# Optimization experiments

Measured on AMD Instinct MI355X. Metric: run time of the kernel, lower is better.

The kernel has to match this reference:

```python
import jax, jax.numpy as jnp
import numpy as np
from jax import lax

EPS = 1e-5
GROUPS = 16


def group_norm(x, gamma, beta, g=GROUPS, eps=EPS):
    B, C, H, W = x.shape
    xr = x.reshape(B, g, C // g, H, W)
    mu = xr.mean(axis=(2, 3, 4), keepdims=True)
    var = xr.var(axis=(2, 3, 4), keepdims=True)
    xn = ((xr - mu) / jnp.sqrt(var + eps)).reshape(B, C, H, W)
    return xn * gamma[None, :, None, None] + beta[None, :, None, None]


def silu(x):
    return x * jax.nn.sigmoid(x)


def recurrence(a, b, c, d, x, axis):
    # h_t = a_t*h_{t-1} + b_t*x_t ; y_t = c_t*h_t + d_t*x_t, scanned along `axis`.
    mv = lambda t: jnp.moveaxis(t, axis, 0)
    def step(h, inp):
        at, bt, ct, dt, xt = inp
        h = at * h + bt * xt
        return h, ct * h + dt * xt
    xs = tuple(map(mv, (a, b, c, d, x)))
    h0 = jnp.zeros_like(xs[4][0])
    _, ys = lax.scan(step, h0, xs)
    return jnp.moveaxis(ys, 0, axis)


def dir_scan(x, wd, bd, axis, flip):
    # Conv1d(c,4c,1) over the scan sequence == pointwise channel linear on NCHW.
    xin = jnp.flip(x, axis) if flip else x
    coeff = jnp.einsum('oc,bchw->bohw', wd, xin) + bd[None, :, None, None]
    C = x.shape[1]
    a, b, c, d = (coeff[:, i * C:(i + 1) * C] for i in range(4))
    a = jax.nn.sigmoid(a)
    y = recurrence(a, b, c, d, xin, axis)
    return jnp.flip(y, axis) if flip else y


def setup_inputs() -> dict:
    key = jax.random.key(0)
    ks = jax.random.split(key, 10)
    B, C, H, W = 4, 128, 128, 128
    s = 1.0 / np.sqrt(C)
    inp = {
        'x': jax.random.normal(ks[0], (B, C, H, W), jnp.float32),
        'w_in': jax.random.normal(ks[1], (C, C), jnp.float32) * s,
        'gn1_gamma': jnp.ones((C,), jnp.float32),
        'gn1_beta': jnp.zeros((C,), jnp.float32),
        'w_gate': jax.random.normal(ks[2], (C, C), jnp.float32) * s,
        'b_gate': jax.random.normal(ks[3], (C,), jnp.float32) * 0.1,
        'dyn_w': jax.random.normal(ks[4], (4, 4 * C, C), jnp.float32) * s,
        'dyn_b': jax.random.normal(ks[5], (4, 4 * C), jnp.float32) * 0.1,
        'dw_kernel': jax.random.normal(ks[6], (C, 1, 3, 3), jnp.float32) * (1.0 / 3.0),
        'w_out': jax.random.normal(ks[7], (C, C), jnp.float32) * s,
        'gn2_gamma': jnp.ones((C,), jnp.float32),
        'gn2_beta': jnp.zeros((C,), jnp.float32),
    }
    return inp


def reference(x, w_in, gn1_gamma, gn1_beta, w_gate, b_gate, dyn_w, dyn_b,
              dw_kernel, w_out, gn2_gamma, gn2_beta):
    C = x.shape[1]
    # in_proj: 1x1 conv (no bias) -> GroupNorm -> SiLU
    xp = jnp.einsum('oc,bchw->bohw', w_in, x)
    xp = silu(group_norm(xp, gn1_gamma, gn1_beta))
    # 4-directional dynamic selective scans
    y_lr = dir_scan(xp, dyn_w[0], dyn_b[0], axis=3, flip=False)
    y_rl = dir_scan(xp, dyn_w[1], dyn_b[1], axis=3, flip=True)
    y_tb = dir_scan(xp, dyn_w[2], dyn_b[2], axis=2, flip=False)
    y_bt = dir_scan(xp, dyn_w[3], dyn_b[3], axis=2, flip=True)
    fused = 0.25 * (y_lr + y_rl + y_tb + y_bt)
    # gate: 1x1 conv + bias -> sigmoid, applied to projected x
    gate = jax.nn.sigmoid(jnp.einsum('oc,bchw->bohw', w_gate, xp)
                          + b_gate[None, :, None, None])
    z = fused * gate
    # out_proj: depthwise 3x3 -> 1x1 conv -> GroupNorm -> SiLU
    z = lax.conv_general_dilated(z, dw_kernel, (1, 1), ((1, 1), (1, 1)),
                                 feature_group_count=C,
                                 dimension_numbers=('NCHW', 'OIHW', 'NCHW'))
    z = jnp.einsum('oc,bchw->bohw', w_out, z)
    return silu(group_norm(z, gn2_gamma, gn2_beta))
```

## Files before the change

### kernel.cpp

```cpp
#include <hip/hip_runtime.h>
#include <math.h>

#define B_ 4
#define C_ 128
#define HW_ 16384
#define P_ 65536
#define S_ 8388608
#define CPG 8

typedef unsigned short u16;
typedef __attribute__((ext_vector_type(8))) short short8;
typedef __attribute__((ext_vector_type(4))) float f32x4;

__device__ __forceinline__ float sigmoidf_(float x){ return 1.f/(1.f+__expf(-x)); }
__device__ __forceinline__ float siluf_(float x){ return x*sigmoidf_(x); }
__device__ __forceinline__ u16 f2bf(float f){
  unsigned x = __float_as_uint(f);
  return (u16)((x + 0x7fffu + ((x >> 16) & 1u)) >> 16);
}
__device__ __forceinline__ float b2f(u16 u){ return __uint_as_float(((unsigned)u) << 16); }

__global__ __launch_bounds__(256) void prep_kernel(const float* __restrict__ dyn_w,
    const float* __restrict__ dyn_b, const float* __restrict__ w_gate,
    const float* __restrict__ w_out, const float* __restrict__ w_in,
    u16* __restrict__ wfrag, float* __restrict__ bperm, u16* __restrict__ wgbf,
    u16* __restrict__ wobf, u16* __restrict__ wibf, float* __restrict__ stats)
{
  int idx = blockIdx.x*256 + threadIdx.x;
  if (idx < 262144) {
    int e = idx & 7, lane = (idx >> 3) & 63, kk = (idx >> 9) & 3;
    int ct = (idx >> 11) & 31, d = idx >> 16;
    int m = lane & 15, kg = lane >> 4;
    int col = ct*16 + m;
    int c = col >> 2, f = col & 3;
    int k = kk*32 + kg*8 + e;
    wfrag[idx] = f2bf(dyn_w[(size_t)((d*512) + f*128 + c)*128 + k]);
  } else if (idx < 264192) {
    int i2 = idx - 262144;
    int op = i2 & 511, d = i2 >> 9;
    bperm[i2] = dyn_b[d*512 + (op & 3)*128 + (op >> 2)];
  } else if (idx < 280576) {
    wgbf[idx - 264192] = f2bf(w_gate[idx - 264192]);
  } else if (idx < 296960) {
    wobf[idx - 280576] = f2bf(w_out[idx - 280576]);
  } else if (idx < 313344) {
    wibf[idx - 296960] = f2bf(w_in[idx - 296960]);
  } else if (idx < 313600) {
    stats[idx - 313344] = 0.f;
  }
}

__global__ __launch_bounds__(256) void xpose(const float* __restrict__ x,
    u16* __restrict__ xT)
{
  __shared__ u16 tile[32*132];
  int b = blockIdx.y;
  int p0 = blockIdx.x << 5;
  int t = threadIdx.x;
  const float* xb = x + ((size_t)b << 21);
  #pragma unroll
  for (int i = 0; i < 16; ++i) {
    int idx = i*256 + t;
    int c = idx >> 5, pp = idx & 31;
    tile[pp*132 + c] = f2bf(xb[(size_t)c*HW_ + p0 + pp]);
  }
  __syncthreads();
  u16* ob = xT + ((size_t)b << 21) + ((size_t)p0 << 7);
  #pragma unroll
  for (int i = 0; i < 2; ++i) {
    int slot = i*256 + t;
    int pp = slot >> 4, j = slot & 15;
    uint2 v0 = *(const uint2*)((const char*)tile + pp*264 + j*16);
    uint2 v1 = *(const uint2*)((const char*)tile + pp*264 + j*16 + 8);
    uint4 o; o.x = v0.x; o.y = v0.y; o.z = v1.x; o.w = v1.y;
    *(uint4*)(ob + (pp << 7) + (j << 3)) = o;
  }
}

template<int BIAS, int SIG>
__global__ __launch_bounds__(256) void mfma_nt128(const u16* __restrict__ X,
    const u16* __restrict__ Wm, const float* __restrict__ bias, u16* __restrict__ Out)
{
  __shared__ __align__(16) u16 st[64*136];
  int t = threadIdx.x;
  int wv = t >> 6, lane = t & 63;
  int m = lane & 15, kg = lane >> 4;
  int pt = blockIdx.x << 6;

  short8 Af[4][4];
  #pragma unroll
  for (int rt = 0; rt < 4; ++rt) {
    const u16* ar = X + ((size_t)(pt + rt*16 + m) << 7) + kg*8;
    #pragma unroll
    for (int kk = 0; kk < 4; ++kk)
      Af[rt][kk] = *(const short8*)(ar + kk*32);
  }
  #pragma unroll
  for (int ct2 = 0; ct2 < 2; ++ct2) {
    int ot = wv*32 + ct2*16;
    const u16* wr = Wm + ((size_t)(ot + m) << 7) + kg*8;
    short8 Bf[4];
    #pragma unroll
    for (int kk = 0; kk < 4; ++kk)
      Bf[kk] = *(const short8*)(wr + kk*32);
    f32x4 acc[4];
    #pragma unroll
    for (int rt = 0; rt < 4; ++rt) acc[rt] = (f32x4){0.f,0.f,0.f,0.f};
    #pragma unroll
    for (int rt = 0; rt < 4; ++rt)
      #pragma unroll
      for (int kk = 0; kk < 4; ++kk)
        acc[rt] = __builtin_amdgcn_mfma_f32_16x16x32_bf16(Af[rt][kk], Bf[kk], acc[rt], 0, 0, 0);
    float bv = BIAS ? bias[ot + m] : 0.f;
    #pragma unroll
    for (int rt = 0; rt < 4; ++rt) {
      #pragma unroll
      for (int r = 0; r < 4; ++r) {
        float v = acc[rt][r] + bv;
        if (SIG) v = sigmoidf_(v);
        st[(rt*16 + kg*4 + r)*136 + ot + m] = f2bf(v);
      }
    }
  }
  __syncthreads();
  #pragma unroll
  for (int i = 0; i < 4; ++i) {
    int slot = i*256 + t;
    int row = slot >> 4, j = slot & 15;
    short8 v = *(const short8*)(st + row*136 + (j << 3));
    *(short8*)(Out + ((size_t)(pt + row) << 7) + (j << 3)) = v;
  }
}

#define PRODUCE(NT, bufv, chunkv)  do { \
  int posg_ = (chunkv)*16 + m; int swp_ = (posg_ & 7) << 4; \
  short8 Bfr[4]; \
  _Pragma("unroll") for (int kk = 0; kk < 4; ++kk) \
    Bfr[kk] = *(const short8*)((char*)xs + posg_*256 + (((kk<<6)+(kg<<4)) ^ swp_)); \
  _Pragma("unroll") for (int ti = 0; ti < NT; ++ti) { \
    f32x4 acc = (f32x4){0.f,0.f,0.f,0.f}; \
    _Pragma("unroll") for (int kk = 0; kk < 4; ++kk) \
      acc = __builtin_amdgcn_mfma_f32_16x16x32_bf16(Af[ti][kk], Bfr[kk], acc, 0, 0, 0); \
    int colL_ = (tbase + ti)*16 + (kg<<2); \
    unsigned lo_ = (unsigned)f2bf(acc[0]) | ((unsigned)f2bf(acc[1])<<16); \
    unsigned hi_ = (unsigned)f2bf(acc[2]) | ((unsigned)f2bf(acc[3])<<16); \
    int byte_ = (((bufv)*2 + dw)<<14) + (m<<10) + ((colL_<<1) ^ ((m&7)<<4)); \
    *(uint2*)((char*)cs + byte_) = make_uint2(lo_, hi_); \
  } } while(0)

#define SCAN_STEP(s) { \
  float ar = b2f((u16)(cw[s].x & 0xffffu)) + bv.x; \
  float br = b2f((u16)(cw[s].x >> 16)) + bv.y; \
  float cr = b2f((u16)(cw[s].y & 0xffffu)) + bv.z; \
  float dr = b2f((u16)(cw[s].y >> 16)) + bv.w; \
  float aa = sigmoidf_(ar); \
  h = aa*h + br*xf[s]; \
  yv[s] = cr*h + dr*xf[s]; }

template<int AXISW, int PART>
__global__ __launch_bounds__(512, 2) void scan_fused(const u16* __restrict__ Abf,
    const u16* __restrict__ Wf, const float* __restrict__ bias,
    u16* __restrict__ fusedP)
{
  __shared__ __align__(16) u16 xs[128*128];
  __shared__ __align__(16) u16 cs[2][2][16*512];
  __shared__ __align__(16) u16 ysL[128*128];
  int line = blockIdx.x;
  int b = line >> 7, l = line & 127;
  int t = threadIdx.x;
  int wv = t >> 6, lane = t & 63;
  int m = lane & 15, kg = lane >> 4;
  int dw = (wv >> 1) & 1;

  #pragma unroll
  for (int i = 0; i < 4; ++i) {
    int idx = i*512 + t;
    int pos = idx >> 4, j = idx & 15;
    size_t row = AXISW ? ((size_t)(b<<14) + (l<<7) + pos)
                       : ((size_t)(b<<14) + (pos<<7) + l);
    short8 v = *(const short8*)(Abf + (row<<7) + (j<<3));
    int byte = pos*256 + ((j*16) ^ ((pos&7)<<4));
    *(short8*)((char*)xs + byte) = v;
  }

  if (wv < 4) {
    int tbase = (wv & 1) * 4;
    short8 Af[4][4];
    #pragma unroll
    for (int ti = 0; ti < 4; ++ti)
      #pragma unroll
      for (int kk = 0; kk < 4; ++kk)
        Af[ti][kk] = *(const short8*)(Wf + (size_t)(((dw*32 + tbase + ti)*4 + kk)*64 + lane)*8);
    __syncthreads();
    PRODUCE(4, 0, dw ? 7 : 0);
    __syncthreads();

    int sd = dw;
    int sc = ((wv & 1) << 6) + lane;
    float4 bv = *(const float4*)(bias + (sd << 9) + (sc << 2));
    float h = 0.f;

    #pragma unroll 1
    for (int k = 0; k < 8; ++k) {
      if (k < 7) PRODUCE(4, (k+1)&1, dw ? (6-k) : (k+1));
      int chunk = sd ? (7-k) : k;
      int csb = (((k&1)*2 + sd) << 14);
      uint2 cw[16];
      #pragma unroll
      for (int s = 0; s < 16; ++s)
        cw[s] = *(const uint2*)((char*)cs + csb + (s<<10) + ((sc<<3) ^ ((s&7)<<4)));
      float xf[16];
      #pragma unroll
      for (int s = 0; s < 16; ++s) {
        int pos = (chunk<<4) + s;
        xf[s] = b2f(*(const u16*)((char*)xs + pos*256 + ((sc<<1) ^ ((s&7)<<4))));
      }
      float yv[16];
      __builtin_amdgcn_s_setprio(1);
      if (sd == 0) {
        #pragma unroll
        for (int s = 0; s < 16; ++s) SCAN_STEP(s)
      } else {
        #pragma unroll
        for (int s = 15; s >= 0; --s) SCAN_STEP(s)
      }
      __builtin_amdgcn_s_setprio(0);
      u16* yrow = ysL + (chunk << 11) + sc;
      if (k <= 3) {
        #pragma unroll
        for (int s = 0; s < 16; ++s) yrow[s << 7] = f2bf(0.25f*yv[s]);
      } else {
        #pragma unroll
        for (int s = 0; s < 16; ++s) {
          float o = b2f(yrow[s << 7]);
          yrow[s << 7] = f2bf(o + 0.25f*yv[s]);
        }
      }
      __syncthreads();
    }
  } else {
    int tbase = 8 + (wv & 1) * 12;
    short8 Af[12][4];
    #pragma unroll
    for (int ti = 0; ti < 12; ++ti)
      #pragma unroll
      for (int kk = 0; kk < 4; ++kk)
        Af[ti][kk] = *(const short8*)(Wf + (size_t)(((dw*32 + tbase + ti)*4 + kk)*64 + lane)*8);
    __syncthreads();
    PRODUCE(12, 0, dw ? 7 : 0);
    __syncthreads();
    #pragma unroll 1
    for (int k = 0; k < 8; ++k) {
      if (k < 7) PRODUCE(12, (k+1)&1, dw ? (6-k) : (k+1));
      __syncthreads();
    }
  }

  #pragma unroll
  for (int r = 0; r < 4; ++r) {
    int slot = r*512 + t;
    int pos = slot >> 4, j = slot & 15;
    short8 v = *(const short8*)(ysL + (pos << 7) + (j << 3));
    size_t rowg = AXISW ? ((size_t)(b<<14) + (l<<7) + pos)
                        : ((size_t)(b<<14) + (pos<<7) + l);
    u16* op = fusedP + (rowg << 7) + (j << 3);
    if (PART) {
      short8 o = *(const short8*)op;
      short8 rr;
      #pragma unroll
      for (int i = 0; i < 8; ++i) rr[i] = (short)f2bf(b2f((u16)v[i]) + b2f((u16)o[i]));
      *(short8*)op = rr;
    } else {
      *(short8*)op = v;
    }
  }
}

__global__ __launch_bounds__(256) void gn_stats_bf(const u16* __restrict__ X,
    float* __restrict__ stats)
{
  int bg = blockIdx.x, chunk = blockIdx.y;
  int b = bg >> 4, g = bg & 15;
  int t = threadIdx.x;
  int c = t & 7, pr = t >> 3;
  const u16* base = X + ((size_t)b << 21) + (g << 3) + c;
  int p0 = chunk << 10;
  float s = 0.f, s2 = 0.f;
  for (int i = 0; i < 32; ++i) {
    float v = b2f(base[(size_t)(p0 + (i << 5) + pr) << 7]);
    s += v; s2 += v*v;
  }
  #pragma unroll
  for (int off = 32; off; off >>= 1) { s += __shfl_down(s, off); s2 += __shfl_down(s2, off); }
  __shared__ float ls[8];
  int wv = t >> 6, lane = t & 63;
  if (lane == 0) { ls[wv] = s; ls[4 + wv] = s2; }
  __syncthreads();
  if (t == 0) {
    atomicAdd(&stats[bg], ls[0]+ls[1]+ls[2]+ls[3]);
    atomicAdd(&stats[64+bg], ls[4]+ls[5]+ls[6]+ls[7]);
  }
}

__global__ __launch_bounds__(256) void gn_apply(const u16* __restrict__ X,
    const float* __restrict__ stats, const float* __restrict__ gamma,
    const float* __restrict__ beta, u16* __restrict__ Xb)
{
  int i4 = blockIdx.x*256 + threadIdx.x;
  size_t base = (size_t)i4 << 2;
  int c4 = (int)(base & 127);
  size_t p = base >> 7;
  int b = (int)(p >> 14);
  int g = c4 >> 3;
  const float cnt = (float)(CPG*HW_);
  float mu = stats[b*16+g]/cnt;
  float var = stats[64+b*16+g]/cnt - mu*mu;
  float rs = rsqrtf(var + 1e-5f);
  ushort4 v = *(const ushort4*)(X + base);
  ushort4 o;
  o.x = f2bf(siluf_((b2f(v.x)-mu)*rs*gamma[c4+0]+beta[c4+0]));
  o.y = f2bf(siluf_((b2f(v.y)-mu)*rs*gamma[c4+1]+beta[c4+1]));
  o.z = f2bf(siluf_((b2f(v.z)-mu)*rs*gamma[c4+2]+beta[c4+2]));
  o.w = f2bf(siluf_((b2f(v.w)-mu)*rs*gamma[c4+3]+beta[c4+3]));
  *(ushort4*)(Xb + base) = o;
}

__global__ __launch_bounds__(256) void dwconv(const u16* __restrict__ Z,
    const u16* __restrict__ G, const float* __restrict__ K9, u16* __restrict__ Outp)
{
  __shared__ float kk[1152];
  int t = threadIdx.x;
  for (int i = t; i < 1152; i += 256) kk[i] = K9[i];
  __syncthreads();
  int i4 = blockIdx.x*256 + t;
  size_t base = (size_t)i4 << 2;
  int c0 = (int)(base & 127);
  size_t p = base >> 7;
  int w = (int)(p & 127), h = (int)((p >> 7) & 127), b = (int)(p >> 14);
  float4 acc = make_float4(0.f,0.f,0.f,0.f);
  #pragma unroll
  for (int di = 0; di < 3; ++di) {
    int hy = h + di - 1;
    if ((unsigned)hy > 127u) continue;
    #pragma unroll
    for (int dj = 0; dj < 3; ++dj) {
      int wx = w + dj - 1;
      if ((unsigned)wx > 127u) continue;
      size_t p2 = ((size_t)b << 14) + (hy << 7) + wx;
      ushort4 zv = *(const ushort4*)(Z + (p2 << 7) + c0);
      ushort4 gv = *(const ushort4*)(G + (p2 << 7) + c0);
      int o = di*3 + dj;
      acc.x += b2f(zv.x) * b2f(gv.x) * kk[c0*9 + o];
      acc.y += b2f(zv.y) * b2f(gv.y) * kk[(c0+1)*9 + o];
      acc.z += b2f(zv.z) * b2f(gv.z) * kk[(c0+2)*9 + o];
      acc.w += b2f(zv.w) * b2f(gv.w) * kk[(c0+3)*9 + o];
    }
  }
  ushort4 ov;
  ov.x = f2bf(acc.x); ov.y = f2bf(acc.y); ov.z = f2bf(acc.z); ov.w = f2bf(acc.w);
  *(ushort4*)(Outp + base) = ov;
}

__global__ __launch_bounds__(256) void gn_final(const u16* __restrict__ Z,
    const float* __restrict__ stats, const float* __restrict__ gamma,
    const float* __restrict__ beta, float* __restrict__ out)
{
  __shared__ float ls[32][129];
  int w0 = blockIdx.x << 5, hh = blockIdx.y, b = blockIdx.z;
  size_t p0 = ((size_t)b << 14) + (hh << 7) + w0;
  int t = threadIdx.x;
  const float cnt = (float)(CPG*HW_);
  #pragma unroll
  for (int i = 0; i < 4; ++i) {
    int l = t + i*256;
    int row = l >> 5, c4 = (l & 31) << 2;
    ushort4 v = *(const ushort4*)(Z + ((p0 + row) << 7) + c4);
    int g = c4 >> 3;
    float mu = stats[b*16+g]/cnt;
    float var = stats[64+b*16+g]/cnt - mu*mu;
    float rs = rsqrtf(var + 1e-5f);
    float vals[4] = {b2f(v.x), b2f(v.y), b2f(v.z), b2f(v.w)};
    #pragma unroll
    for (int j = 0; j < 4; ++j) {
      float nv = (vals[j]-mu)*rs*gamma[c4+j] + beta[c4+j];
      ls[row][c4+j] = siluf_(nv);
    }
  }
  __syncthreads();
  int ww = t & 31, c0 = t >> 5;
  #pragma unroll
  for (int cc = c0; cc < 128; cc += 8) {
    out[(((size_t)(b*128 + cc)) << 14) + (hh << 7) + (w0 + ww)] = ls[ww][cc];
  }
}

extern "C" void kernel_launch(void* const* d_in, const int* in_sizes, int n_in,
                              void* d_out, int out_size, void* d_ws, size_t ws_size,
                              hipStream_t stream)
{
  (void)in_sizes; (void)n_in; (void)out_size; (void)ws_size;
  const float* x      = (const float*)d_in[0];
  const float* w_in   = (const float*)d_in[1];
  const float* g1g    = (const float*)d_in[2];
  const float* g1b    = (const float*)d_in[3];
  const float* w_gate = (const float*)d_in[4];
  const float* b_gate = (const float*)d_in[5];
  const float* dyn_w  = (const float*)d_in[6];
  const float* dyn_b  = (const float*)d_in[7];
  const float* dwk    = (const float*)d_in[8];
  const float* w_out  = (const float*)d_in[9];
  const float* g2g    = (const float*)d_in[10];
  const float* g2b    = (const float*)d_in[11];
  float* out = (float*)d_out;

  char* p = (char*)d_ws;
  u16*   xT     = (u16*)p;              p += (size_t)S_*2;
  u16*   xpr    = (u16*)p;              p += (size_t)S_*2;
  u16*   Abf    = (u16*)p;              p += (size_t)S_*2;
  u16*   fusedP = (u16*)p;              p += (size_t)S_*2;
  u16*   Gbf    = (u16*)p;              p += (size_t)S_*2;
  u16*   wfrag  = (u16*)p;              p += (size_t)262144*2;
  u16*   wgbf   = (u16*)p;              p += (size_t)16384*2;
  u16*   wobf   = (u16*)p;              p += (size_t)16384*2;
  u16*   wibf   = (u16*)p;              p += (size_t)16384*2;
  float* bperm  = (float*)p;            p += (size_t)2048*4;
  float* stats  = (float*)p;            p += (size_t)256*4;
  u16*   Zdw    = xT;
  u16*   Zout   = xpr;

  prep_kernel<<<1225, 256, 0, stream>>>(dyn_w, dyn_b, w_gate, w_out, w_in,
                                        wfrag, bperm, wgbf, wobf, wibf, stats);
  xpose<<<dim3(512, 4), 256, 0, stream>>>(x, xT);
  mfma_nt128<0,0><<<1024, 256, 0, stream>>>(xT, wibf, nullptr, xpr);
  gn_stats_bf<<<dim3(64, 16), 256, 0, stream>>>(xpr, stats);
  gn_apply<<<8192, 256, 0, stream>>>(xpr, stats, g1g, g1b, Abf);

  scan_fused<1,0><<<512, 512, 0, stream>>>(Abf, wfrag, bperm, fusedP);
  scan_fused<0,1><<<512, 512, 0, stream>>>(Abf, wfrag + 131072, bperm + 1024, fusedP);

  mfma_nt128<1,1><<<1024, 256, 0, stream>>>(Abf, wgbf, b_gate, Gbf);
  dwconv<<<8192, 256, 0, stream>>>(fusedP, Gbf, dwk, Zdw);
  mfma_nt128<0,0><<<1024, 256, 0, stream>>>(Zdw, wobf, nullptr, Zout);
  gn_stats_bf<<<dim3(64, 16), 256, 0, stream>>>(Zout, stats + 128);
  gn_final<<<dim3(4, 128, 4), 256, 0, stream>>>(Zout, stats + 128, g2g, g2b, out);
}
```

Before: 236.2 us.

## Fuse input transpose into in-proj MFMA and vectorize GroupNorm stats reduction

Removes the separate xpose kernel. The in-projection GEMM now reads the fp32 NCHW input directly, converts it to bf16 in registers, and builds its MFMA A fragments from strided channel loads. This drops one full bf16 intermediate write and read plus a kernel launch. GroupNorm statistics now use contiguous 16-byte loads over position-major data with per-group shuffle and shared-atomic reduction, replacing strided scalar loads. The strided fp32 gathers in the in-proj kernel may coalesce poorly across lanes.

```diff
diff --git a/kernel.cpp b/kernel.cpp
--- a/kernel.cpp
+++ b/kernel.cpp
@@ -50,30 +50,61 @@
   }
 }
 
-__global__ __launch_bounds__(256) void xpose(const float* __restrict__ x,
-    u16* __restrict__ xT)
-{
-  __shared__ u16 tile[32*132];
-  int b = blockIdx.y;
-  int p0 = blockIdx.x << 5;
-  int t = threadIdx.x;
+__global__ __launch_bounds__(256) void mfma_inproj(const float* __restrict__ x,
+    const u16* __restrict__ Wm, u16* __restrict__ Out)
+{
+  __shared__ __align__(16) u16 st[64*136];
+  int t = threadIdx.x;
+  int wv = t >> 6, lane = t & 63;
+  int m = lane & 15, kg = lane >> 4;
+  int pt = blockIdx.x << 6;
+  int b = blockIdx.x >> 8;
+  int hw0 = (blockIdx.x & 255) << 6;
   const float* xb = x + ((size_t)b << 21);
-  #pragma unroll
-  for (int i = 0; i < 16; ++i) {
-    int idx = i*256 + t;
-    int c = idx >> 5, pp = idx & 31;
-    tile[pp*132 + c] = f2bf(xb[(size_t)c*HW_ + p0 + pp]);
-  }
-  __syncthreads();
-  u16* ob = xT + ((size_t)b << 21) + ((size_t)p0 << 7);
-  #pragma unroll
-  for (int i = 0; i < 2; ++i) {
+
+  short8 Af[4][4];
+  #pragma unroll
+  for (int rt = 0; rt < 4; ++rt) {
+    int pos = hw0 + rt*16 + m;
+    #pragma unroll
+    for (int kk = 0; kk < 4; ++kk) {
+      short8 f;
+      #pragma unroll
+      for (int e = 0; e < 8; ++e)
+        f[e] = (short)f2bf(xb[(size_t)(kk*32 + kg*8 + e)*HW_ + pos]);
+      Af[rt][kk] = f;
+    }
+  }
+  #pragma unroll
+  for (int ct2 = 0; ct2 < 2; ++ct2) {
+    int ot = wv*32 + ct2*16;
+    const u16* wr = Wm + ((size_t)(ot + m) << 7) + kg*8;
+    short8 Bf[4];
+    #pragma unroll
+    for (int kk = 0; kk < 4; ++kk)
+      Bf[kk] = *(const short8*)(wr + kk*32);
+    f32x4 acc[4];
+    #pragma unroll
+    for (int rt = 0; rt < 4; ++rt) acc[rt] = (f32x4){0.f,0.f,0.f,0.f};
+    #pragma unroll
+    for (int rt = 0; rt < 4; ++rt)
+      #pragma unroll
+      for (int kk = 0; kk < 4; ++kk)
+        acc[rt] = __builtin_amdgcn_mfma_f32_16x16x32_bf16(Af[rt][kk], Bf[kk], acc[rt], 0, 0, 0);
+    #pragma unroll
+    for (int rt = 0; rt < 4; ++rt) {
+      #pragma unroll
+      for (int r = 0; r < 4; ++r)
+        st[(rt*16 + kg*4 + r)*136 + ot + m] = f2bf(acc[rt][r]);
+    }
+  }
+  __syncthreads();
+  #pragma unroll
+  for (int i = 0; i < 4; ++i) {
     int slot = i*256 + t;
-    int pp = slot >> 4, j = slot & 15;
-    uint2 v0 = *(const uint2*)((const char*)tile + pp*264 + j*16);
-    uint2 v1 = *(const uint2*)((const char*)tile + pp*264 + j*16 + 8);
-    uint4 o; o.x = v0.x; o.y = v0.y; o.z = v1.x; o.w = v1.y;
-    *(uint4*)(ob + (pp << 7) + (j << 3)) = o;
+    int row = slot >> 4, j = slot & 15;
+    short8 v = *(const short8*)(st + row*136 + (j << 3));
+    *(short8*)(Out + ((size_t)(pt + row) << 7) + (j << 3)) = v;
   }
 }
 
@@ -279,27 +310,26 @@
 __global__ __launch_bounds__(256) void gn_stats_bf(const u16* __restrict__ X,
     float* __restrict__ stats)
 {
-  int bg = blockIdx.x, chunk = blockIdx.y;
-  int b = bg >> 4, g = bg & 15;
-  int t = threadIdx.x;
-  int c = t & 7, pr = t >> 3;
-  const u16* base = X + ((size_t)b << 21) + (g << 3) + c;
-  int p0 = chunk << 10;
-  float s = 0.f, s2 = 0.f;
-  for (int i = 0; i < 32; ++i) {
-    float v = b2f(base[(size_t)(p0 + (i << 5) + pr) << 7]);
-    s += v; s2 += v*v;
-  }
-  #pragma unroll
-  for (int off = 32; off; off >>= 1) { s += __shfl_down(s, off); s2 += __shfl_down(s2, off); }
-  __shared__ float ls[8];
-  int wv = t >> 6, lane = t & 63;
-  if (lane == 0) { ls[wv] = s; ls[4 + wv] = s2; }
-  __syncthreads();
-  if (t == 0) {
-    atomicAdd(&stats[bg], ls[0]+ls[1]+ls[2]+ls[3]);
-    atomicAdd(&stats[64+bg], ls[4]+ls[5]+ls[6]+ls[7]);
-  }
+  int b = blockIdx.x, chunk = blockIdx.y;
+  const u16* base = X + ((size_t)b << 21) + ((size_t)chunk << 15);
+  int t = threadIdx.x;
+  float s = 0.f, q = 0.f;
+  #pragma unroll 4
+  for (int it = 0; it < 16; ++it) {
+    short8 v = *(const short8*)(base + it*2048 + t*8);
+    #pragma unroll
+    for (int e = 0; e < 8; ++e) { float f = b2f((u16)v[e]); s += f; q += f*f; }
+  }
+  s += __shfl_xor(s, 16); q += __shfl_xor(q, 16);
+  s += __shfl_xor(s, 32); q += __shfl_xor(q, 32);
+  __shared__ float sg[32];
+  if (t < 32) sg[t] = 0.f;
+  __syncthreads();
+  int lane = t & 63;
+  if (lane < 16) { atomicAdd(&sg[lane], s); atomicAdd(&sg[16 + lane], q); }
+  __syncthreads();
+  if (t < 16) atomicAdd(&stats[b*16 + t], sg[t]);
+  else if (t < 32) atomicAdd(&stats[64 + b*16 + (t - 16)], sg[t]);
 }
 
 __global__ __launch_bounds__(256) void gn_apply(const u16* __restrict__ X,
@@ -414,7 +444,7 @@
   float* out = (float*)d_out;
 
   char* p = (char*)d_ws;
-  u16*   xT     = (u16*)p;              p += (size_t)S_*2;
+  u16*   Zbuf   = (u16*)p;              p += (size_t)S_*2;
   u16*   xpr    = (u16*)p;              p += (size_t)S_*2;
   u16*   Abf    = (u16*)p;              p += (size_t)S_*2;
   u16*   fusedP = (u16*)p;              p += (size_t)S_*2;
@@ -425,14 +455,13 @@
   u16*   wibf   = (u16*)p;              p += (size_t)16384*2;
   float* bperm  = (float*)p;            p += (size_t)2048*4;
   float* stats  = (float*)p;            p += (size_t)256*4;
-  u16*   Zdw    = xT;
+  u16*   Zdw    = Zbuf;
   u16*   Zout   = xpr;
 
   prep_kernel<<<1225, 256, 0, stream>>>(dyn_w, dyn_b, w_gate, w_out, w_in,
                                         wfrag, bperm, wgbf, wobf, wibf, stats);
-  xpose<<<dim3(512, 4), 256, 0, stream>>>(x, xT);
-  mfma_nt128<0,0><<<1024, 256, 0, stream>>>(xT, wibf, nullptr, xpr);
-  gn_stats_bf<<<dim3(64, 16), 256, 0, stream>>>(xpr, stats);
+  mfma_inproj<<<1024, 256, 0, stream>>>(x, wibf, xpr);
+  gn_stats_bf<<<dim3(4, 64), 256, 0, stream>>>(xpr, stats);
   gn_apply<<<8192, 256, 0, stream>>>(xpr, stats, g1g, g1b, Abf);
 
   scan_fused<1,0><<<512, 512, 0, stream>>>(Abf, wfrag, bperm, fusedP);
@@ -441,6 +470,6 @@
   mfma_nt128<1,1><<<1024, 256, 0, stream>>>(Abf, wgbf, b_gate, Gbf);
   dwconv<<<8192, 256, 0, stream>>>(fusedP, Gbf, dwk, Zdw);
   mfma_nt128<0,0><<<1024, 256, 0, stream>>>(Zdw, wobf, nullptr, Zout);
-  gn_stats_bf<<<dim3(64, 16), 256, 0, stream>>>(Zout, stats + 128);
+  gn_stats_bf<<<dim3(4, 64), 256, 0, stream>>>(Zout, stats + 128);
   gn_final<<<dim3(4, 128, 4), 256, 0, stream>>>(Zout, stats + 128, g2g, g2b, out);
 }
```

Result: faster. 199.1 us (-15.7%).
